# Kernel optimization log

Hardware: AMD Instinct MI355X
Metric: run time of the kernel (lower is better)

## Reference

```python
import jax, jax.numpy as jnp
import numpy as np

NUM_NODES = 100000
NUM_RELS = 500
DIM = 64          # input_dim == hidden_dim == output_dim
NUM_EDGES = 1_000_000
LEAKY_SLOPE = 0.01  # torch F.leaky_relu default


def _linear_params(key, fin, fout):
    # torch nn.Linear default init: U(-1/sqrt(fin), 1/sqrt(fin))
    kw, kb = jax.random.split(key)
    s = 1.0 / np.sqrt(fin)
    W = jax.random.uniform(kw, (fout, fin), minval=-s, maxval=s, dtype=jnp.float32)
    b = jax.random.uniform(kb, (fout,), minval=-s, maxval=s, dtype=jnp.float32)
    return W, b


def setup_inputs() -> dict:
    key = jax.random.key(0)
    ks = jax.random.split(key, 12)
    src_idx = jax.random.randint(ks[0], (NUM_EDGES,), 0, NUM_NODES, dtype=jnp.int32)
    dst_idx = jax.random.randint(ks[1], (NUM_EDGES,), 0, NUM_NODES, dtype=jnp.int32)
    rel_idx = jax.random.randint(ks[2], (NUM_EDGES,), 0, NUM_RELS, dtype=jnp.int32)
    ent_embed = jax.random.normal(ks[3], (NUM_NODES, DIM), dtype=jnp.float32)
    rel_embed = jax.random.normal(ks[4], (NUM_RELS, DIM), dtype=jnp.float32)
    W_ent, b_ent = _linear_params(ks[5], DIM, DIM)          # fc_ent
    W_relL, b_relL = _linear_params(ks[6], DIM, DIM)        # fc_rel
    W_rel2, b_rel2 = _linear_params(ks[7], DIM, DIM)        # fc_rel2
    W_rel3, b_rel3 = _linear_params(ks[8], 3 * DIM, DIM)    # fc_rel3
    W_a, b_a = _linear_params(ks[9], DIM, 1)                # a
    W_fc, b_fc = _linear_params(ks[10], 3 * DIM, DIM)       # fc
    return {
        "ent_embed": ent_embed, "rel_embed": rel_embed,
        "W_ent": W_ent, "b_ent": b_ent,
        "W_relL": W_relL, "b_relL": b_relL,
        "W_rel2": W_rel2, "b_rel2": b_rel2,
        "W_rel3": W_rel3, "b_rel3": b_rel3,
        "W_a": W_a, "b_a": b_a,
        "W_fc": W_fc, "b_fc": b_fc,
        "src_idx": src_idx, "dst_idx": dst_idx, "rel_idx": rel_idx,
    }


def reference(ent_embed, rel_embed, W_ent, b_ent, W_relL, b_relL,
              W_rel2, b_rel2, W_rel3, b_rel3, W_a, b_a, W_fc, b_fc,
              src_idx, dst_idx, rel_idx):
    # --- per-edge projections (first=True path: lookup from learned tables) ---
    src = ent_embed[src_idx] @ W_ent.T + b_ent            # [E, D]
    dst = ent_embed[dst_idx] @ W_ent.T + b_ent            # [E, D]
    rel = rel_embed[rel_idx] @ W_relL.T + b_relL          # [E, D]

    # --- edge message c and unnormalized attention b ---
    c = jnp.concatenate([src, dst, rel], axis=1) @ W_fc.T + b_fc   # [E, D]
    logits = jax.nn.leaky_relu((c @ W_a.T + b_a)[:, 0], LEAKY_SLOPE)  # [E]
    b = jnp.exp(logits)                                    # [E] (original uses plain exp)

    # --- scatter-softmax over edges grouped by source node ---
    b_sum = jax.ops.segment_sum(b, src_idx, num_segments=NUM_NODES)  # [N]
    alpha = b / b_sum[src_idx]                             # [E]

    # --- attention-weighted neighbor aggregation ---
    h_ent = jax.ops.segment_sum(alpha[:, None] * c, src_idx,
                                num_segments=NUM_NODES)    # [N, D]

    # --- relation pooling: mean over edges of each relation ---
    rel2 = rel @ W_rel2.T + b_rel2                         # [E, D]
    feats = jnp.concatenate([h_ent[src_idx], h_ent[dst_idx], rel2], axis=1)  # [E, 3D]
    sums = jax.ops.segment_sum(feats, rel_idx, num_segments=NUM_RELS)        # [R, 3D]
    counts = jax.ops.segment_sum(jnp.ones_like(b), rel_idx, num_segments=NUM_RELS)
    mean = sums / jnp.maximum(counts, 1.0)[:, None]        # [R, 3D]

    h_rel = mean @ W_rel3.T + b_rel3                       # [R, D]
    return (h_ent, h_rel)
```

## Files before the change

kernel.cpp:

```cpp
#include <hip/hip_runtime.h>
#include <math.h>

#define N_NODES 100000
#define N_RELS  500
#define DIM     64
#define N_EDGES 1000000
#define SLOPE   0.01f
#define RSUB    16
#define SC_EDGES 2048
#define NB_E    489
#define NBKT    196
#define BSH     9
#define NROWS   (N_RELS + NBKT)
#define BMAX    5632

__device__ __forceinline__ unsigned short f2bf(float f) {
    unsigned int u = __float_as_uint(f);
    u += 0x7FFFu + ((u >> 16) & 1u);
    return (unsigned short)(u >> 16);
}
__device__ __forceinline__ float bfl(unsigned int u) { return __uint_as_float(u << 16); }
__device__ __forceinline__ float bfh(unsigned int u) { return __uint_as_float(u & 0xFFFF0000u); }

__global__ void k_fold(const float* __restrict__ W_ent, const float* __restrict__ b_ent,
                       const float* __restrict__ W_relL, const float* __restrict__ b_relL,
                       const float* __restrict__ W_rel2, const float* __restrict__ b_rel2,
                       const float* __restrict__ W_fc, const float* __restrict__ b_fc,
                       float* __restrict__ Wcat, float* __restrict__ dcat,
                       float* __restrict__ MW, float* __restrict__ MQ,
                       float* __restrict__ dW, float* __restrict__ dQ) {
    int idx = blockIdx.x * 256 + threadIdx.x;
    if (idx < 8192) {
        int k = idx >> 7;
        int j2 = idx & 127;
        int jj = j2 & 63;
        int off = (j2 >> 6) * 64;
        float s = 0.f;
        for (int i = 0; i < 64; i++) s += W_fc[jj*192 + off + i] * W_ent[i*64 + k];
        Wcat[k*128 + j2] = s;
    } else if (idx < 12288) {
        int rem = idx - 8192;
        int j = rem >> 6, i = rem & 63;
        float s = 0.f;
        for (int k = 0; k < 64; k++) s += W_fc[j*192 + 128 + k] * W_relL[k*64 + i];
        MW[j*64 + i] = s;
    } else if (idx < 16384) {
        int rem = idx - 12288;
        int j = rem >> 6, i = rem & 63;
        float s = 0.f;
        for (int k = 0; k < 64; k++) s += W_rel2[j*64 + k] * W_relL[k*64 + i];
        MQ[j*64 + i] = s;
    } else if (idx < 16512) {
        int j2 = idx - 16384;
        int jj = j2 & 63;
        int off = (j2 >> 6) * 64;
        float s = 0.f;
        for (int i = 0; i < 64; i++) s += b_ent[i] * W_fc[jj*192 + off + i];
        dcat[j2] = s;
    } else if (idx < 16640) {
        int rem = idx - 16512;
        int vec = rem >> 6, j = rem & 63;
        if (vec == 0) {
            float s = b_fc[j];
            for (int k = 0; k < 64; k++) s += b_relL[k] * W_fc[j*192 + 128 + k];
            dW[j] = s;
        } else {
            float s = b_rel2[j];
            for (int k = 0; k < 64; k++) s += b_relL[k] * W_rel2[j*64 + k];
            dQ[j] = s;
        }
    }
}

__global__ __launch_bounds__(256) void k_node(const float* __restrict__ ent,
        const float* __restrict__ Wcat, const float* __restrict__ dcat,
        const float* __restrict__ W_a,
        float* __restrict__ Uout, unsigned short* __restrict__ V16,
        float* __restrict__ us, float* __restrict__ vs) {
    __shared__ float sA[64][68];
    __shared__ float sW[64][128];
    int t = threadIdx.x;
    int tile0 = blockIdx.x * 64;
    for (int i = t; i < 2048; i += 256)
        ((float4*)sW)[i] = ((const float4*)Wcat)[i];
    for (int f = t; f < 1024; f += 256) {
        int n = f >> 4, k4 = f & 15;
        float4 v4 = (tile0 + n < N_NODES)
            ? ((const float4*)(ent + (size_t)(tile0 + n) * 64))[k4]
            : make_float4(0.f, 0.f, 0.f, 0.f);
        *(float4*)&sA[n][k4 * 4] = v4;
    }
    __syncthreads();

    int ng = t >> 4;
    int jg = t & 15;
    int n0 = ng * 4;
    int j0 = jg * 8;

    float4 d0 = *(const float4*)(dcat + j0);
    float4 d1 = *(const float4*)(dcat + j0 + 4);
    float acc[4][8];
    #pragma unroll
    for (int a = 0; a < 4; a++) {
        acc[a][0] = d0.x; acc[a][1] = d0.y; acc[a][2] = d0.z; acc[a][3] = d0.w;
        acc[a][4] = d1.x; acc[a][5] = d1.y; acc[a][6] = d1.z; acc[a][7] = d1.w;
    }

    #pragma unroll 4
    for (int k = 0; k < 64; k++) {
        float4 w0 = *(const float4*)&sW[k][j0];
        float4 w1 = *(const float4*)&sW[k][j0 + 4];
        float e0 = sA[n0][k], e1 = sA[n0+1][k], e2 = sA[n0+2][k], e3 = sA[n0+3][k];
        float e[4] = {e0, e1, e2, e3};
        #pragma unroll
        for (int a = 0; a < 4; a++) {
            acc[a][0] += e[a] * w0.x; acc[a][1] += e[a] * w0.y;
            acc[a][2] += e[a] * w0.z; acc[a][3] += e[a] * w0.w;
            acc[a][4] += e[a] * w1.x; acc[a][5] += e[a] * w1.y;
            acc[a][6] += e[a] * w1.z; acc[a][7] += e[a] * w1.w;
        }
    }

    int jw = j0 & 63;
    float4 wa0 = *(const float4*)(W_a + jw);
    float4 wa1 = *(const float4*)(W_a + jw + 4);
    float part[4];
    #pragma unroll
    for (int a = 0; a < 4; a++) {
        part[a] = acc[a][0]*wa0.x + acc[a][1]*wa0.y + acc[a][2]*wa0.z + acc[a][3]*wa0.w
                + acc[a][4]*wa1.x + acc[a][5]*wa1.y + acc[a][6]*wa1.z + acc[a][7]*wa1.w;
    }
    #pragma unroll
    for (int m = 1; m <= 4; m <<= 1) {
        #pragma unroll
        for (int a = 0; a < 4; a++) part[a] += __shfl_xor(part[a], m, 64);
    }
    if ((jg & 7) == 0) {
        float* sv = (jg < 8) ? us : vs;
        #pragma unroll
        for (int a = 0; a < 4; a++)
            if (tile0 + n0 + a < N_NODES) sv[tile0 + n0 + a] = part[a];
    }

    #pragma unroll
    for (int a = 0; a < 4; a++) {
        int n = tile0 + n0 + a;
        if (n >= N_NODES) break;
        if (jg < 8) {
            float4 o0 = make_float4(acc[a][0], acc[a][1], acc[a][2], acc[a][3]);
            float4 o1 = make_float4(acc[a][4], acc[a][5], acc[a][6], acc[a][7]);
            float* base = Uout + (size_t)n * 64 + j0;
            *(float4*)(base) = o0;
            *(float4*)(base + 4) = o1;
        } else {
            uint4 pv;
            pv.x = (unsigned int)f2bf(acc[a][0]) | ((unsigned int)f2bf(acc[a][1]) << 16);
            pv.y = (unsigned int)f2bf(acc[a][2]) | ((unsigned int)f2bf(acc[a][3]) << 16);
            pv.z = (unsigned int)f2bf(acc[a][4]) | ((unsigned int)f2bf(acc[a][5]) << 16);
            pv.w = (unsigned int)f2bf(acc[a][6]) | ((unsigned int)f2bf(acc[a][7]) << 16);
            *(uint4*)(V16 + (size_t)n * 64 + (j0 - 64)) = pv;
        }
    }
}

__global__ __launch_bounds__(256, 2) void k_relproj(const float* __restrict__ relE,
        const float* __restrict__ MW, const float* __restrict__ MQ,
        const float* __restrict__ dW, const float* __restrict__ dQ,
        const float* __restrict__ W_a,
        unsigned short* __restrict__ Wr16, float* __restrict__ Qr, float* __restrict__ wsr) {
    int lane = threadIdx.x & 63;
    int wv = threadIdx.x >> 6;
    float mw[64], mq[64];
    #pragma unroll
    for (int i = 0; i < 64; i++) { mw[i] = MW[lane*64 + i]; mq[i] = MQ[lane*64 + i]; }
    float dw = dW[lane], dq = dQ[lane], wa = W_a[lane];
    int r = blockIdx.x * 4 + wv;
    if (r >= N_RELS) return;
    float e = relE[(size_t)r * 64 + lane];
    float w = dw, q = dq;
    #pragma unroll
    for (int i = 0; i < 64; i++) {
        float ei = __shfl(e, i, 64);
        w += ei * mw[i];
        q += ei * mq[i];
    }
    Wr16[(size_t)r * 64 + lane] = f2bf(w);
    Qr[(size_t)r * 64 + lane] = q;
    float tw = w * wa;
    #pragma unroll
    for (int o = 32; o; o >>= 1) tw += __shfl_xor(tw, o, 64);
    if (lane == 0) wsr[r] = tw;
}

__global__ void k_zero(int* __restrict__ a, int n) {
    int g = blockIdx.x * 256 + threadIdx.x;
    if (g < n) a[g] = 0;
}

__global__ __launch_bounds__(256) void k_hist(const int* __restrict__ src, const int* __restrict__ rel,
        int* __restrict__ cnt_rel, int* __restrict__ bucket_cnt, int* __restrict__ blkhist) {
    __shared__ int lcntR[N_RELS];
    __shared__ int lcntS[NBKT];
    int t = threadIdx.x;
    for (int r = t; r < N_RELS; r += 256) lcntR[r] = 0;
    for (int b = t; b < NBKT; b += 256) lcntS[b] = 0;
    __syncthreads();
    int base = blockIdx.x * SC_EDGES;
    if (base + SC_EDGES <= N_EDGES) {
        int e0 = base + t * 8;
        int4 sa = *(const int4*)(src + e0);
        int4 sb = *(const int4*)(src + e0 + 4);
        int4 ra = *(const int4*)(rel + e0);
        int4 rb = *(const int4*)(rel + e0 + 4);
        atomicAdd(&lcntS[sa.x >> BSH], 1); atomicAdd(&lcntS[sa.y >> BSH], 1);
        atomicAdd(&lcntS[sa.z >> BSH], 1); atomicAdd(&lcntS[sa.w >> BSH], 1);
        atomicAdd(&lcntS[sb.x >> BSH], 1); atomicAdd(&lcntS[sb.y >> BSH], 1);
        atomicAdd(&lcntS[sb.z >> BSH], 1); atomicAdd(&lcntS[sb.w >> BSH], 1);
        atomicAdd(&lcntR[ra.x], 1); atomicAdd(&lcntR[ra.y], 1);
        atomicAdd(&lcntR[ra.z], 1); atomicAdd(&lcntR[ra.w], 1);
        atomicAdd(&lcntR[rb.x], 1); atomicAdd(&lcntR[rb.y], 1);
        atomicAdd(&lcntR[rb.z], 1); atomicAdd(&lcntR[rb.w], 1);
    } else {
        for (int g = base + t; g < N_EDGES; g += 256) {
            atomicAdd(&lcntS[src[g] >> BSH], 1);
            atomicAdd(&lcntR[rel[g]], 1);
        }
    }
    __syncthreads();
    for (int r = t; r < N_RELS; r += 256) {
        int c = lcntR[r];
        blkhist[(size_t)r * NB_E + blockIdx.x] = c;
        if (c) atomicAdd(&cnt_rel[r], c);
    }
    for (int b = t; b < NBKT; b += 256) {
        int c = lcntS[b];
        blkhist[(size_t)(N_RELS + b) * NB_E + blockIdx.x] = c;
        if (c) atomicAdd(&bucket_cnt[b], c);
    }
}

__global__ void k_scan_two(const int* __restrict__ cnt_rel, const int* __restrict__ bucket_cnt,
                           int* __restrict__ starts) {
    __shared__ int tot[256];
    int t = threadIdx.x;
    const int* cnt = blockIdx.x ? bucket_cnt : cnt_rel;
    int n = blockIdx.x ? NBKT : N_RELS;
    int* out = starts + (blockIdx.x ? N_RELS : 0);
    int myv[4];
    int mySum = 0;
    for (int q = 0; q < 4; q++) {
        int g = t * 4 + q;
        int v = (g < n) ? cnt[g] : 0;
        myv[q] = v; mySum += v;
    }
    tot[t] = mySum;
    __syncthreads();
    for (int o = 1; o < 256; o <<= 1) {
        int u = (t >= o) ? tot[t - o] : 0;
        __syncthreads();
        tot[t] += u;
        __syncthreads();
    }
    int run = tot[t] - mySum;
    for (int q = 0; q < 4; q++) {
        int g = t * 4 + q;
        if (g < n) out[g] = run;
        run += myv[q];
    }
}

__global__ __launch_bounds__(256) void k_scan_relblk(const int* __restrict__ starts,
        const int* __restrict__ blkhist, int* __restrict__ blkbase) {
    int lane = threadIdx.x & 63;
    int row = (blockIdx.x * 256 + threadIdx.x) >> 6;
    if (row >= NROWS) return;
    int run = starts[row];
    for (int base = 0; base < NB_E; base += 64) {
        int b = base + lane;
        int v = (b < NB_E) ? blkhist[(size_t)row * NB_E + b] : 0;
        int x = v;
        #pragma unroll
        for (int o = 1; o < 64; o <<= 1) {
            int y = __shfl_up(x, o, 64);
            if (lane >= o) x += y;
        }
        if (b < NB_E) blkbase[(size_t)row * NB_E + b] = run + (x - v);
        run += __shfl(x, 63, 64);
    }
}

__global__ __launch_bounds__(256) void k_scatter(const int* __restrict__ src, const int* __restrict__ dst,
        const int* __restrict__ rel, const int* __restrict__ blkbase,
        int2* __restrict__ pay_rel, int* __restrict__ stg_a, int* __restrict__ stg_b) {
    __shared__ int lbaseR[N_RELS];
    __shared__ int loffR[N_RELS];
    __shared__ int lbaseS[NBKT];
    __shared__ int loffS[NBKT];
    int t = threadIdx.x;
    for (int r = t; r < N_RELS; r += 256) {
        lbaseR[r] = blkbase[(size_t)r * NB_E + blockIdx.x];
        loffR[r] = 0;
    }
    for (int b = t; b < NBKT; b += 256) {
        lbaseS[b] = blkbase[(size_t)(N_RELS + b) * NB_E + blockIdx.x];
        loffS[b] = 0;
    }
    __syncthreads();
    int base = blockIdx.x * SC_EDGES;
    if (base + SC_EDGES <= N_EDGES) {
        int e0 = base + t * 8;
        int4 sa = *(const int4*)(src + e0);
        int4 sb = *(const int4*)(src + e0 + 4);
        int4 da = *(const int4*)(dst + e0);
        int4 db = *(const int4*)(dst + e0 + 4);
        int4 ra = *(const int4*)(rel + e0);
        int4 rb = *(const int4*)(rel + e0 + 4);
        int s[8] = {sa.x, sa.y, sa.z, sa.w, sb.x, sb.y, sb.z, sb.w};
        int d[8] = {da.x, da.y, da.z, da.w, db.x, db.y, db.z, db.w};
        int r8[8] = {ra.x, ra.y, ra.z, ra.w, rb.x, rb.y, rb.z, rb.w};
        int p[8], q[8];
        #pragma unroll
        for (int j = 0; j < 8; j++) q[j] = lbaseR[r8[j]] + atomicAdd(&loffR[r8[j]], 1);
        #pragma unroll
        for (int j = 0; j < 8; j++) p[j] = lbaseS[s[j] >> BSH] + atomicAdd(&loffS[s[j] >> BSH], 1);
        #pragma unroll
        for (int j = 0; j < 8; j++) pay_rel[q[j]] = make_int2(s[j], d[j]);
        #pragma unroll
        for (int j = 0; j < 8; j++) stg_a[p[j]] = d[j];
        #pragma unroll
        for (int j = 0; j < 8; j++) stg_b[p[j]] = ((s[j] & 511) << 9) | r8[j];
    } else {
        for (int g = base + t; g < N_EDGES; g += 256) {
            int s = src[g], d = dst[g], r = rel[g];
            int q = lbaseR[r] + atomicAdd(&loffR[r], 1);
            pay_rel[q] = make_int2(s, d);
            int sb2 = s >> BSH;
            int p = lbaseS[sb2] + atomicAdd(&loffS[sb2], 1);
            stg_a[p] = d;
            stg_b[p] = ((s & 511) << 9) | r;
        }
    }
}

__global__ __launch_bounds__(256) void k_sortb(const int* __restrict__ stg_a,
        const int* __restrict__ stg_b, const int* __restrict__ starts,
        const int* __restrict__ bucket_cnt, int2* __restrict__ pay_src,
        int* __restrict__ start_src, int* __restrict__ cnt_src) {
    __shared__ int hist[512];
    __shared__ int lstart[512];
    __shared__ int loff[512];
    __shared__ int tot[256];
    __shared__ int2 lpay[BMAX];
    int bkt = blockIdx.x;
    int base = starts[N_RELS + bkt];
    int n = bucket_cnt[bkt];
    int t = threadIdx.x;
    hist[t] = 0; hist[t + 256] = 0;
    __syncthreads();
    for (int i = t; i < n; i += 256)
        atomicAdd(&hist[stg_b[base + i] >> 9], 1);
    __syncthreads();
    int v0 = hist[t * 2], v1 = hist[t * 2 + 1];
    int mySum = v0 + v1;
    tot[t] = mySum;
    __syncthreads();
    for (int o = 1; o < 256; o <<= 1) {
        int u = (t >= o) ? tot[t - o] : 0;
        __syncthreads();
        tot[t] += u;
        __syncthreads();
    }
    int run = tot[t] - mySum;
    lstart[t * 2] = run;
    lstart[t * 2 + 1] = run + v0;
    loff[t * 2] = 0;
    loff[t * 2 + 1] = 0;
    int node0 = bkt * 512 + t * 2;
    if (node0 < N_NODES) { start_src[node0] = base + run; cnt_src[node0] = v0; }
    if (node0 + 1 < N_NODES) { start_src[node0 + 1] = base + run + v0; cnt_src[node0 + 1] = v1; }
    __syncthreads();
    bool fits = (n <= BMAX);
    for (int i = t; i < n; i += 256) {
        int bb = stg_b[base + i];
        int d = stg_a[base + i];
        int lo = bb >> 9;
        int2 pr = make_int2(d, bb & 511);
        int pos = lstart[lo] + atomicAdd(&loff[lo], 1);
        if (fits) lpay[pos] = pr;
        else pay_src[base + pos] = pr;
    }
    __syncthreads();
    if (fits)
        for (int i = t; i < n; i += 256)
            pay_src[base + i] = lpay[i];
}

__global__ __launch_bounds__(256) void k_attn(const int2* __restrict__ pay,
        const int* __restrict__ start_src, const int* __restrict__ cnt_src,
        const float* __restrict__ us, const float* __restrict__ vs,
        const float* __restrict__ wsr, const unsigned short* __restrict__ V16,
        const unsigned short* __restrict__ Wr16, const float* __restrict__ b_a_p,
        float* __restrict__ h, unsigned short* __restrict__ h16) {
    int lane = threadIdx.x & 63;
    int wv = threadIdx.x >> 6;
    int n = blockIdx.x * 4 + wv;
    if (n >= N_NODES) return;
    int st = start_src[n];
    int cnt = cnt_src[n];
    if (cnt == 0) {
        h[(size_t)n * 64 + lane] = 0.f;
        if (lane < 8) *(uint4*)(h16 + (size_t)n * 64 + lane * 8) = make_uint4(0,0,0,0);
        return;
    }
    float ba = b_a_p[0];
    float usn = us[n];

    if (cnt <= 64) {
        int2 pe = (lane < cnt) ? pay[st + lane] : make_int2(0, 0);
        float bexp = 0.f;
        if (lane < cnt) {
            float s = usn + vs[pe.x] + wsr[pe.y] + ba;
            s = s > 0.f ? s : SLOPE * s;
            bexp = expf(s);
        }
        float bp = bexp;
        #pragma unroll
        for (int o = 32; o; o >>= 1) bp += __shfl_xor(bp, o, 64);
        float inv = 1.f / bp;
        int sub = lane >> 3;
        int li = lane & 7;
        float a[8] = {0.f,0.f,0.f,0.f,0.f,0.f,0.f,0.f};
        int groups = (cnt + 7) >> 3;
        for (int g = 0; g < groups; g++) {
            int esel = 8 * g + sub;
            float be = __shfl(bexp, esel, 64);
            int de = __shfl(pe.x, esel, 64);
            int re = __shfl(pe.y, esel, 64);
            uint4 vv = *(const uint4*)(V16 + (size_t)de * 64 + li * 8);
            uint4 ww = *(const uint4*)(Wr16 + (size_t)re * 64 + li * 8);
            a[0] += be * (bfl(vv.x) + bfl(ww.x)); a[1] += be * (bfh(vv.x) + bfh(ww.x));
            a[2] += be * (bfl(vv.y) + bfl(ww.y)); a[3] += be * (bfh(vv.y) + bfh(ww.y));
            a[4] += be * (bfl(vv.z) + bfl(ww.z)); a[5] += be * (bfh(vv.z) + bfh(ww.z));
            a[6] += be * (bfl(vv.w) + bfl(ww.w)); a[7] += be * (bfh(vv.w) + bfh(ww.w));
        }
        #pragma unroll
        for (int m = 8; m <= 32; m <<= 1) {
            #pragma unroll
            for (int d = 0; d < 8; d++) a[d] += __shfl_xor(a[d], m, 64);
        }
        if (lane < 8) {
            float* hp = h + (size_t)n * 64 + lane * 8;
            float o[8];
            #pragma unroll
            for (int d = 0; d < 8; d++) o[d] = hp[d] + a[d] * inv;
            float4 o0 = make_float4(o[0], o[1], o[2], o[3]);
            float4 o1 = make_float4(o[4], o[5], o[6], o[7]);
            *(float4*)hp = o0;
            *(float4*)(hp + 4) = o1;
            uint4 pv;
            pv.x = (unsigned int)f2bf(o[0]) | ((unsigned int)f2bf(o[1]) << 16);
            pv.y = (unsigned int)f2bf(o[2]) | ((unsigned int)f2bf(o[3]) << 16);
            pv.z = (unsigned int)f2bf(o[4]) | ((unsigned int)f2bf(o[5]) << 16);
            pv.w = (unsigned int)f2bf(o[6]) | ((unsigned int)f2bf(o[7]) << 16);
            *(uint4*)(h16 + (size_t)n * 64 + lane * 8) = pv;
        }
        return;
    }

    float bp = 0.f;
    for (int k = lane; k < cnt; k += 64) {
        int2 p = pay[st + k];
        float s = usn + vs[p.x] + wsr[p.y] + ba;
        s = s > 0.f ? s : SLOPE * s;
        bp += expf(s);
    }
    #pragma unroll
    for (int o = 32; o; o >>= 1) bp += __shfl_xor(bp, o, 64);
    float inv = 1.f / bp;
    float acc = 0.f;
    for (int k = 0; k < cnt; k++) {
        int2 p = pay[st + k];
        float s = usn + vs[p.x] + wsr[p.y] + ba;
        s = s > 0.f ? s : SLOPE * s;
        float b = expf(s);
        float vv = bfl((unsigned int)V16[(size_t)p.x * 64 + lane] << 16 >> 16 << 16);
        vv = __uint_as_float((unsigned int)V16[(size_t)p.x * 64 + lane] << 16);
        float wv2 = __uint_as_float((unsigned int)Wr16[(size_t)p.y * 64 + lane] << 16);
        acc += b * (vv + wv2);
    }
    float u = h[(size_t)n * 64 + lane];
    float o = u + acc * inv;
    h[(size_t)n * 64 + lane] = o;
    h16[(size_t)n * 64 + lane] = f2bf(o);
}

__global__ __launch_bounds__(256) void k_relpool(const int2* __restrict__ pay,
        const int* __restrict__ start_rel, const int* __restrict__ cnt_rel,
        const unsigned short* __restrict__ h16, float* __restrict__ acc_rel) {
    int r = blockIdx.x / RSUB;
    int sub = blockIdx.x % RSUB;
    int st = start_rel[r];
    int cnt = cnt_rel[r];
    int t = threadIdx.x;
    int j = t >> 4;
    int side = (t >> 3) & 1;
    int li = t & 7;

    int chunk = (cnt + RSUB - 1) / RSUB;
    int k0 = sub * chunk;
    int k1 = min(k0 + chunk, cnt);
    int len = k1 - k0;

    float a[8] = {0.f,0.f,0.f,0.f,0.f,0.f,0.f,0.f};
    if (len > 0) {
        int steps = (len + 31) >> 5;
        int mA = j, mB = j + 16;
        bool vA = mA < len, vB = mB < len;
        int2 pA = vA ? pay[st + k0 + mA] : make_int2(0, 0);
        int2 pB = vB ? pay[st + k0 + mB] : make_int2(0, 0);
        for (int it = 0; it < steps; it++) {
            int nA = mA + 32, nB = mB + 32;
            bool wA = (it + 1 < steps) && (nA < len);
            bool wB = (it + 1 < steps) && (nB < len);
            int2 qA = wA ? pay[st + k0 + nA] : make_int2(0, 0);
            int2 qB = wB ? pay[st + k0 + nB] : make_int2(0, 0);
            int idxA = side ? pA.y : pA.x;
            int idxB = side ? pB.y : pB.x;
            uint4 hA = *(const uint4*)(h16 + (size_t)idxA * 64 + li * 8);
            uint4 hB = *(const uint4*)(h16 + (size_t)idxB * 64 + li * 8);
            if (vA) {
                a[0] += bfl(hA.x); a[1] += bfh(hA.x); a[2] += bfl(hA.y); a[3] += bfh(hA.y);
                a[4] += bfl(hA.z); a[5] += bfh(hA.z); a[6] += bfl(hA.w); a[7] += bfh(hA.w);
            }
            if (vB) {
                a[0] += bfl(hB.x); a[1] += bfh(hB.x); a[2] += bfl(hB.y); a[3] += bfh(hB.y);
                a[4] += bfl(hB.z); a[5] += bfh(hB.z); a[6] += bfl(hB.w); a[7] += bfh(hB.w);
            }
            pA = qA; pB = qB; mA = nA; mB = nB; vA = wA; vB = wB;
        }
    }
    __shared__ float red[256][8];
    #pragma unroll
    for (int d = 0; d < 8; d++) red[t][d] = a[d];
    __syncthreads();
    #pragma unroll
    for (int off = 128; off >= 16; off >>= 1) {
        if (t < off) {
            #pragma unroll
            for (int d = 0; d < 8; d++) red[t][d] += red[t + off][d];
        }
        __syncthreads();
    }
    if (t < 16) {
        int sd = (t >> 3) & 1;
        int ll = t & 7;
        float* dstp = &acc_rel[r * 128 + sd * 64 + ll * 8];
        #pragma unroll
        for (int d = 0; d < 8; d++) atomicAdd(dstp + d, red[t][d]);
    }
}

__global__ void k_relfin(const float* __restrict__ acc_rel, const int* __restrict__ cnt_rel,
                         const float* __restrict__ Qr, const float* __restrict__ W_rel3,
                         const float* __restrict__ b_rel3, float* __restrict__ out) {
    int g = blockIdx.x * 256 + threadIdx.x;
    if (g >= N_RELS * 64) return;
    int r = g >> 6;
    int j = g & 63;
    int cnt = cnt_rel[r];
    float invc = 1.f / (float)(cnt > 0 ? cnt : 1);
    float s = b_rel3[j];
    for (int k = 0; k < 128; k++) s += acc_rel[r * 128 + k] * invc * W_rel3[j * 192 + k];
    if (cnt > 0)
        for (int k = 0; k < 64; k++) s += Qr[r * 64 + k] * W_rel3[j * 192 + 128 + k];
    out[g] = s;
}

extern "C" void kernel_launch(void* const* d_in, const int* in_sizes, int n_in,
                              void* d_out, int out_size, void* d_ws, size_t ws_size,
                              hipStream_t stream) {
    const float* ent    = (const float*)d_in[0];
    const float* relE   = (const float*)d_in[1];
    const float* W_ent  = (const float*)d_in[2];
    const float* b_ent  = (const float*)d_in[3];
    const float* W_relL = (const float*)d_in[4];
    const float* b_relL = (const float*)d_in[5];
    const float* W_rel2 = (const float*)d_in[6];
    const float* b_rel2 = (const float*)d_in[7];
    const float* W_rel3 = (const float*)d_in[8];
    const float* b_rel3 = (const float*)d_in[9];
    const float* W_a    = (const float*)d_in[10];
    const float* b_a    = (const float*)d_in[11];
    const float* W_fc   = (const float*)d_in[12];
    const float* b_fc   = (const float*)d_in[13];
    const int* src = (const int*)d_in[14];
    const int* dst = (const int*)d_in[15];
    const int* rel = (const int*)d_in[16];
    float* out = (float*)d_out;

    char* ws = (char*)d_ws;
    size_t off = 0;
    auto alloc = [&](size_t bytes) -> void* {
        void* p = ws + off;
        off += (bytes + 255) & ~(size_t)255;
        return p;
    };
    float* Wcat = (float*)alloc(8192 * 4);
    float* dcat = (float*)alloc(128 * 4);
    float* MW  = (float*)alloc(4096 * 4);
    float* MQ  = (float*)alloc(4096 * 4);
    float* dW  = (float*)alloc(64 * 4);
    float* dQ  = (float*)alloc(64 * 4);
    unsigned short* V16 = (unsigned short*)alloc((size_t)N_NODES * 64 * 2);
    unsigned short* h16 = (unsigned short*)alloc((size_t)N_NODES * 64 * 2);
    float* us  = (float*)alloc((size_t)N_NODES * 4);
    float* vs  = (float*)alloc((size_t)N_NODES * 4);
    unsigned short* Wr16 = (unsigned short*)alloc((size_t)N_RELS * 64 * 2);
    float* Qr  = (float*)alloc((size_t)N_RELS * 64 * 4);
    float* wsr = (float*)alloc((size_t)N_RELS * 4);
    int* cnt_src   = (int*)alloc((size_t)N_NODES * 4);
    int* start_src = (int*)alloc((size_t)N_NODES * 4);
    int* cnts      = (int*)alloc((size_t)NROWS * 4);
    int* starts    = (int*)alloc((size_t)NROWS * 4);
    int* blkhist   = (int*)alloc((size_t)NROWS * NB_E * 4);
    int* blkbase   = (int*)alloc((size_t)NROWS * NB_E * 4);
    int* stg_a     = (int*)alloc((size_t)N_EDGES * 4);
    int* stg_b     = (int*)alloc((size_t)N_EDGES * 4);
    int2* pay_src  = (int2*)alloc((size_t)N_EDGES * 8);
    int2* pay_rel  = (int2*)alloc((size_t)N_EDGES * 8);
    float* acc_rel = (float*)alloc((size_t)N_RELS * 128 * 4);

    int* cnt_rel    = cnts;
    int* bucket_cnt = cnts + N_RELS;

    k_zero<<<(NROWS + 255) / 256, 256, 0, stream>>>(cnts, NROWS);
    k_zero<<<(N_RELS * 128 + 255) / 256, 256, 0, stream>>>((int*)acc_rel, N_RELS * 128);

    k_fold<<<65, 256, 0, stream>>>(W_ent, b_ent, W_relL, b_relL, W_rel2, b_rel2,
                                   W_fc, b_fc, Wcat, dcat, MW, MQ, dW, dQ);
    k_node<<<(N_NODES + 63) / 64, 256, 0, stream>>>(ent, Wcat, dcat, W_a, out, V16, us, vs);
    k_relproj<<<125, 256, 0, stream>>>(relE, MW, MQ, dW, dQ, W_a, Wr16, Qr, wsr);
    k_hist<<<NB_E, 256, 0, stream>>>(src, rel, cnt_rel, bucket_cnt, blkhist);
    k_scan_two<<<2, 256, 0, stream>>>(cnt_rel, bucket_cnt, starts);
    k_scan_relblk<<<(NROWS * 64 + 255) / 256, 256, 0, stream>>>(starts, blkhist, blkbase);
    k_scatter<<<NB_E, 256, 0, stream>>>(src, dst, rel, blkbase, pay_rel, stg_a, stg_b);
    k_sortb<<<NBKT, 256, 0, stream>>>(stg_a, stg_b, starts, bucket_cnt,
                                      pay_src, start_src, cnt_src);
    k_attn<<<N_NODES / 4, 256, 0, stream>>>(pay_src, start_src, cnt_src,
                                            us, vs, wsr, V16, Wr16, b_a, out, h16);
    k_relpool<<<N_RELS * RSUB, 256, 0, stream>>>(pay_rel, starts, cnt_rel, h16, acc_rel);
    k_relfin<<<(N_RELS * 64 + 255) / 256, 256, 0, stream>>>(acc_rel, cnt_rel, Qr, W_rel3,
                                                            b_rel3, out + (size_t)N_NODES * 64);
}
```

Before: 319.4 us.

## Precompute attention exp weights and per-node sums in sort kernel, pack four nodes per wave

The sort kernel now computes each edge's leaky-relu exp logit and accumulates per-source-node softmax denominators in shared memory, writing a per-edge weight array and a per-node sum array. The attention kernel drops its own logit and reduction pass and just reads those weights. It also handles four nodes per wave (16 lanes each) with two edges in flight per iteration. This should cut idle lanes for low-degree nodes and remove the separate exp pass. The cost is an extra 4 MB weight array plus scattered us/vs/wsr loads inside the sort kernel, and high-degree nodes now get only 16 lanes.

```diff
diff --git a/kernel.cpp b/kernel.cpp
--- a/kernel.cpp
+++ b/kernel.cpp
@@ -344,18 +344,25 @@
 
 __global__ __launch_bounds__(256) void k_sortb(const int* __restrict__ stg_a,
         const int* __restrict__ stg_b, const int* __restrict__ starts,
-        const int* __restrict__ bucket_cnt, int2* __restrict__ pay_src,
-        int* __restrict__ start_src, int* __restrict__ cnt_src) {
+        const int* __restrict__ bucket_cnt,
+        const float* __restrict__ us, const float* __restrict__ vs,
+        const float* __restrict__ wsr, const float* __restrict__ b_a_p,
+        int2* __restrict__ pay_src, float* __restrict__ pay_b,
+        int* __restrict__ start_src, int* __restrict__ cnt_src,
+        float* __restrict__ bsum_arr) {
     __shared__ int hist[512];
     __shared__ int lstart[512];
     __shared__ int loff[512];
     __shared__ int tot[256];
+    __shared__ float lbsum[512];
     __shared__ int2 lpay[BMAX];
     int bkt = blockIdx.x;
     int base = starts[N_RELS + bkt];
     int n = bucket_cnt[bkt];
     int t = threadIdx.x;
+    float ba = b_a_p[0];
     hist[t] = 0; hist[t + 256] = 0;
+    lbsum[t] = 0.f; lbsum[t + 256] = 0.f;
     __syncthreads();
     for (int i = t; i < n; i += 256)
         atomicAdd(&hist[stg_b[base + i] >> 9], 1);
@@ -384,114 +391,105 @@
         int bb = stg_b[base + i];
         int d = stg_a[base + i];
         int lo = bb >> 9;
-        int2 pr = make_int2(d, bb & 511);
         int pos = lstart[lo] + atomicAdd(&loff[lo], 1);
-        if (fits) lpay[pos] = pr;
-        else pay_src[base + pos] = pr;
-    }
-    __syncthreads();
-    if (fits)
-        for (int i = t; i < n; i += 256)
-            pay_src[base + i] = lpay[i];
+        if (fits) {
+            lpay[pos] = make_int2(d, bb);
+        } else {
+            int r = bb & 511;
+            int s = bkt * 512 + lo;
+            float t0 = us[s] + vs[d] + wsr[r] + ba;
+            t0 = t0 > 0.f ? t0 : SLOPE * t0;
+            float b = expf(t0);
+            pay_src[base + pos] = make_int2(d, r);
+            pay_b[base + pos] = b;
+            atomicAdd(&lbsum[lo], b);
+        }
+    }
+    __syncthreads();
+    if (fits) {
+        for (int i = t; i < n; i += 256) {
+            int2 pr = lpay[i];
+            int bb = pr.y;
+            int lo = bb >> 9;
+            int r = bb & 511;
+            int s = bkt * 512 + lo;
+            float t0 = us[s] + vs[pr.x] + wsr[r] + ba;
+            t0 = t0 > 0.f ? t0 : SLOPE * t0;
+            float b = expf(t0);
+            pay_src[base + i] = make_int2(pr.x, r);
+            pay_b[base + i] = b;
+            atomicAdd(&lbsum[lo], b);
+        }
+        __syncthreads();
+    }
+    if (node0 < N_NODES) bsum_arr[node0] = lbsum[t * 2];
+    if (node0 + 1 < N_NODES) bsum_arr[node0 + 1] = lbsum[t * 2 + 1];
 }
 
 __global__ __launch_bounds__(256) void k_attn(const int2* __restrict__ pay,
+        const float* __restrict__ pay_b,
         const int* __restrict__ start_src, const int* __restrict__ cnt_src,
-        const float* __restrict__ us, const float* __restrict__ vs,
-        const float* __restrict__ wsr, const unsigned short* __restrict__ V16,
-        const unsigned short* __restrict__ Wr16, const float* __restrict__ b_a_p,
+        const float* __restrict__ bsum_arr,
+        const unsigned short* __restrict__ V16, const unsigned short* __restrict__ Wr16,
         float* __restrict__ h, unsigned short* __restrict__ h16) {
     int lane = threadIdx.x & 63;
     int wv = threadIdx.x >> 6;
-    int n = blockIdx.x * 4 + wv;
+    int quarter = lane >> 4;
+    int lq = lane & 15;
+    int slot = lq >> 3;
+    int li = lq & 7;
+    int n = blockIdx.x * 16 + wv * 4 + quarter;
     if (n >= N_NODES) return;
     int st = start_src[n];
     int cnt = cnt_src[n];
     if (cnt == 0) {
-        h[(size_t)n * 64 + lane] = 0.f;
-        if (lane < 8) *(uint4*)(h16 + (size_t)n * 64 + lane * 8) = make_uint4(0,0,0,0);
+        if (lq < 8) {
+            float* hp = h + (size_t)n * 64 + lq * 8;
+            *(float4*)hp = make_float4(0.f, 0.f, 0.f, 0.f);
+            *(float4*)(hp + 4) = make_float4(0.f, 0.f, 0.f, 0.f);
+            *(uint4*)(h16 + (size_t)n * 64 + lq * 8) = make_uint4(0, 0, 0, 0);
+        }
         return;
     }
-    float ba = b_a_p[0];
-    float usn = us[n];
-
-    if (cnt <= 64) {
-        int2 pe = (lane < cnt) ? pay[st + lane] : make_int2(0, 0);
-        float bexp = 0.f;
-        if (lane < cnt) {
-            float s = usn + vs[pe.x] + wsr[pe.y] + ba;
-            s = s > 0.f ? s : SLOPE * s;
-            bexp = expf(s);
-        }
-        float bp = bexp;
-        #pragma unroll
-        for (int o = 32; o; o >>= 1) bp += __shfl_xor(bp, o, 64);
-        float inv = 1.f / bp;
-        int sub = lane >> 3;
-        int li = lane & 7;
-        float a[8] = {0.f,0.f,0.f,0.f,0.f,0.f,0.f,0.f};
-        int groups = (cnt + 7) >> 3;
-        for (int g = 0; g < groups; g++) {
-            int esel = 8 * g + sub;
-            float be = __shfl(bexp, esel, 64);
-            int de = __shfl(pe.x, esel, 64);
-            int re = __shfl(pe.y, esel, 64);
-            uint4 vv = *(const uint4*)(V16 + (size_t)de * 64 + li * 8);
-            uint4 ww = *(const uint4*)(Wr16 + (size_t)re * 64 + li * 8);
-            a[0] += be * (bfl(vv.x) + bfl(ww.x)); a[1] += be * (bfh(vv.x) + bfh(ww.x));
-            a[2] += be * (bfl(vv.y) + bfl(ww.y)); a[3] += be * (bfh(vv.y) + bfh(ww.y));
-            a[4] += be * (bfl(vv.z) + bfl(ww.z)); a[5] += be * (bfh(vv.z) + bfh(ww.z));
-            a[6] += be * (bfl(vv.w) + bfl(ww.w)); a[7] += be * (bfh(vv.w) + bfh(ww.w));
-        }
-        #pragma unroll
-        for (int m = 8; m <= 32; m <<= 1) {
-            #pragma unroll
-            for (int d = 0; d < 8; d++) a[d] += __shfl_xor(a[d], m, 64);
-        }
-        if (lane < 8) {
-            float* hp = h + (size_t)n * 64 + lane * 8;
-            float o[8];
-            #pragma unroll
-            for (int d = 0; d < 8; d++) o[d] = hp[d] + a[d] * inv;
-            float4 o0 = make_float4(o[0], o[1], o[2], o[3]);
-            float4 o1 = make_float4(o[4], o[5], o[6], o[7]);
-            *(float4*)hp = o0;
-            *(float4*)(hp + 4) = o1;
-            uint4 pv;
-            pv.x = (unsigned int)f2bf(o[0]) | ((unsigned int)f2bf(o[1]) << 16);
-            pv.y = (unsigned int)f2bf(o[2]) | ((unsigned int)f2bf(o[3]) << 16);
-            pv.z = (unsigned int)f2bf(o[4]) | ((unsigned int)f2bf(o[5]) << 16);
-            pv.w = (unsigned int)f2bf(o[6]) | ((unsigned int)f2bf(o[7]) << 16);
-            *(uint4*)(h16 + (size_t)n * 64 + lane * 8) = pv;
-        }
-        return;
-    }
-
-    float bp = 0.f;
-    for (int k = lane; k < cnt; k += 64) {
-        int2 p = pay[st + k];
-        float s = usn + vs[p.x] + wsr[p.y] + ba;
-        s = s > 0.f ? s : SLOPE * s;
-        bp += expf(s);
-    }
-    #pragma unroll
-    for (int o = 32; o; o >>= 1) bp += __shfl_xor(bp, o, 64);
-    float inv = 1.f / bp;
-    float acc = 0.f;
-    for (int k = 0; k < cnt; k++) {
-        int2 p = pay[st + k];
-        float s = usn + vs[p.x] + wsr[p.y] + ba;
-        s = s > 0.f ? s : SLOPE * s;
-        float b = expf(s);
-        float vv = bfl((unsigned int)V16[(size_t)p.x * 64 + lane] << 16 >> 16 << 16);
-        vv = __uint_as_float((unsigned int)V16[(size_t)p.x * 64 + lane] << 16);
-        float wv2 = __uint_as_float((unsigned int)Wr16[(size_t)p.y * 64 + lane] << 16);
-        acc += b * (vv + wv2);
-    }
-    float u = h[(size_t)n * 64 + lane];
-    float o = u + acc * inv;
-    h[(size_t)n * 64 + lane] = o;
-    h16[(size_t)n * 64 + lane] = f2bf(o);
+    float inv = 1.f / bsum_arr[n];
+    float a[8] = {0.f, 0.f, 0.f, 0.f, 0.f, 0.f, 0.f, 0.f};
+    for (int e = slot; e < cnt; e += 4) {
+        int eB = e + 2;
+        bool vB = eB < cnt;
+        int eBc = vB ? eB : e;
+        float bA = pay_b[st + e];
+        float bB = vB ? pay_b[st + eB] : 0.f;
+        int2 pA = pay[st + e];
+        int2 pB = pay[st + eBc];
+        uint4 vvA = *(const uint4*)(V16 + (size_t)pA.x * 64 + li * 8);
+        uint4 wwA = *(const uint4*)(Wr16 + (size_t)pA.y * 64 + li * 8);
+        uint4 vvB = *(const uint4*)(V16 + (size_t)pB.x * 64 + li * 8);
+        uint4 wwB = *(const uint4*)(Wr16 + (size_t)pB.y * 64 + li * 8);
+        a[0] += bA * (bfl(vvA.x) + bfl(wwA.x)) + bB * (bfl(vvB.x) + bfl(wwB.x));
+        a[1] += bA * (bfh(vvA.x) + bfh(wwA.x)) + bB * (bfh(vvB.x) + bfh(wwB.x));
+        a[2] += bA * (bfl(vvA.y) + bfl(wwA.y)) + bB * (bfl(vvB.y) + bfl(wwB.y));
+        a[3] += bA * (bfh(vvA.y) + bfh(wwA.y)) + bB * (bfh(vvB.y) + bfh(wwB.y));
+        a[4] += bA * (bfl(vvA.z) + bfl(wwA.z)) + bB * (bfl(vvB.z) + bfl(wwB.z));
+        a[5] += bA * (bfh(vvA.z) + bfh(wwA.z)) + bB * (bfh(vvB.z) + bfh(wwB.z));
+        a[6] += bA * (bfl(vvA.w) + bfl(wwA.w)) + bB * (bfl(vvB.w) + bfl(wwB.w));
+        a[7] += bA * (bfh(vvA.w) + bfh(wwA.w)) + bB * (bfh(vvB.w) + bfh(wwB.w));
+    }
+    #pragma unroll
+    for (int d = 0; d < 8; d++) a[d] += __shfl_xor(a[d], 8, 64);
+    if (slot == 0) {
+        float* hp = h + (size_t)n * 64 + li * 8;
+        float o[8];
+        #pragma unroll
+        for (int d = 0; d < 8; d++) o[d] = hp[d] + a[d] * inv;
+        *(float4*)hp = make_float4(o[0], o[1], o[2], o[3]);
+        *(float4*)(hp + 4) = make_float4(o[4], o[5], o[6], o[7]);
+        uint4 pv;
+        pv.x = (unsigned int)f2bf(o[0]) | ((unsigned int)f2bf(o[1]) << 16);
+        pv.y = (unsigned int)f2bf(o[2]) | ((unsigned int)f2bf(o[3]) << 16);
+        pv.z = (unsigned int)f2bf(o[4]) | ((unsigned int)f2bf(o[5]) << 16);
+        pv.w = (unsigned int)f2bf(o[6]) | ((unsigned int)f2bf(o[7]) << 16);
+        *(uint4*)(h16 + (size_t)n * 64 + li * 8) = pv;
+    }
 }
 
 __global__ __launch_bounds__(256) void k_relpool(const int2* __restrict__ pay,
@@ -620,6 +618,7 @@
     float* wsr = (float*)alloc((size_t)N_RELS * 4);
     int* cnt_src   = (int*)alloc((size_t)N_NODES * 4);
     int* start_src = (int*)alloc((size_t)N_NODES * 4);
+    float* bsum    = (float*)alloc((size_t)N_NODES * 4);
     int* cnts      = (int*)alloc((size_t)NROWS * 4);
     int* starts    = (int*)alloc((size_t)NROWS * 4);
     int* blkhist   = (int*)alloc((size_t)NROWS * NB_E * 4);
@@ -627,6 +626,7 @@
     int* stg_a     = (int*)alloc((size_t)N_EDGES * 4);
     int* stg_b     = (int*)alloc((size_t)N_EDGES * 4);
     int2* pay_src  = (int2*)alloc((size_t)N_EDGES * 8);
+    float* pay_b   = (float*)alloc((size_t)N_EDGES * 4);
     int2* pay_rel  = (int2*)alloc((size_t)N_EDGES * 8);
     float* acc_rel = (float*)alloc((size_t)N_RELS * 128 * 4);
 
@@ -645,9 +645,10 @@
     k_scan_relblk<<<(NROWS * 64 + 255) / 256, 256, 0, stream>>>(starts, blkhist, blkbase);
     k_scatter<<<NB_E, 256, 0, stream>>>(src, dst, rel, blkbase, pay_rel, stg_a, stg_b);
     k_sortb<<<NBKT, 256, 0, stream>>>(stg_a, stg_b, starts, bucket_cnt,
-                                      pay_src, start_src, cnt_src);
-    k_attn<<<N_NODES / 4, 256, 0, stream>>>(pay_src, start_src, cnt_src,
-                                            us, vs, wsr, V16, Wr16, b_a, out, h16);
+                                      us, vs, wsr, b_a,
+                                      pay_src, pay_b, start_src, cnt_src, bsum);
+    k_attn<<<(N_NODES + 15) / 16, 256, 0, stream>>>(pay_src, pay_b, start_src, cnt_src,
+                                                    bsum, V16, Wr16, out, h16);
     k_relpool<<<N_RELS * RSUB, 256, 0, stream>>>(pay_rel, starts, cnt_rel, h16, acc_rel);
     k_relfin<<<(N_RELS * 64 + 255) / 256, 256, 0, stream>>>(acc_rel, cnt_rel, Qr, W_rel3,
                                                             b_rel3, out + (size_t)N_NODES * 64);
```

After: 310.3 us. 2.8% less time.
